# Performance work log

Measured on AMD Instinct MI355X. Metric: run time of the kernel, lower is better.

Reference implementation:

```python
import jax, jax.numpy as jnp
import numpy as np

N = 50000      # nodes per graph batch (per siamese side)
E = 500000     # edges per side
F_IN = 128     # input_channels
H = 128        # hidden_channels
OUT = 2        # output_channels
G = 512        # number of graphs in the batch


def setup_inputs() -> dict:
    key = jax.random.key(0)
    ks = jax.random.split(key, 16)

    def lin_w(k, fan_in, shape):
        lim = 1.0 / np.sqrt(fan_in)
        return jax.random.uniform(k, shape, jnp.float32, -lim, lim)

    return {
        "x1": jax.random.normal(ks[0], (N, F_IN), jnp.float32),
        "x2": jax.random.normal(ks[1], (N, F_IN), jnp.float32),
        "edge_index1": jax.random.randint(ks[2], (2, E), 0, N, jnp.int32),
        "edge_index2": jax.random.randint(ks[3], (2, E), 0, N, jnp.int32),
        "batch1": jnp.sort(jax.random.randint(ks[4], (N,), 0, G, jnp.int32)),
        "batch2": jnp.sort(jax.random.randint(ks[5], (N,), 0, G, jnp.int32)),
        "W1": lin_w(ks[6], F_IN, (F_IN, H)), "b1": jnp.zeros((H,), jnp.float32),
        "W2": lin_w(ks[7], H, (H, H)),       "b2": jnp.zeros((H,), jnp.float32),
        "W3": lin_w(ks[8], H, (H, H)),       "b3": jnp.zeros((H,), jnp.float32),
        "Wc1": lin_w(ks[9], 2 * H, (2 * H, 4 * H)), "bc1": jnp.zeros((4 * H,), jnp.float32),
        "Wc2": lin_w(ks[10], 4 * H, (4 * H, 2 * H)), "bc2": jnp.zeros((2 * H,), jnp.float32),
        "Wc3": lin_w(ks[11], 2 * H, (2 * H, OUT)),   "bc3": jnp.zeros((OUT,), jnp.float32),
        "num_graphs": G,
    }


def _gcn_layer(x, W, b, src, dst, dinv):
    # PyG GCNConv: linear transform, then deg^{-1/2} A_hat deg^{-1/2} aggregation + bias
    h = x @ W
    msg = h[src] * (dinv[src] * dinv[dst])[:, None]   # [E+N, H]
    return jax.ops.segment_sum(msg, dst, num_segments=x.shape[0]) + b


def _forward_once(x, edge_index, batch, W1, b1, W2, b2, W3, b3, num_graphs):
    n = x.shape[0]
    loop = jnp.arange(n, dtype=edge_index.dtype)
    src = jnp.concatenate([edge_index[0], loop])      # add self-loops
    dst = jnp.concatenate([edge_index[1], loop])
    deg = jax.ops.segment_sum(jnp.ones_like(dst, dtype=x.dtype), dst, num_segments=n)
    dinv = jax.lax.rsqrt(deg)                          # deg >= 1 due to self-loops
    h = jax.nn.relu(_gcn_layer(x, W1, b1, src, dst, dinv))
    h = jax.nn.relu(_gcn_layer(h, W2, b2, src, dst, dinv))
    h = _gcn_layer(h, W3, b3, src, dst, dinv)
    # global_mean_pool over batch indices
    s = jax.ops.segment_sum(h, batch, num_segments=num_graphs)
    cnt = jax.ops.segment_sum(jnp.ones((n,), x.dtype), batch, num_segments=num_graphs)
    return s / jnp.maximum(cnt, 1.0)[:, None]


def reference(x1, x2, edge_index1, edge_index2, batch1, batch2,
              W1, b1, W2, b2, W3, b3, Wc1, bc1, Wc2, bc2, Wc3, bc3, num_graphs):
    g1 = _forward_once(x1, edge_index1, batch1, W1, b1, W2, b2, W3, b3, num_graphs)
    g2 = _forward_once(x2, edge_index2, batch2, W1, b1, W2, b2, W3, b3, num_graphs)
    z = jnp.concatenate([g1, g2], axis=1)             # [G, 2H]
    z = jax.nn.relu(z @ Wc1 + bc1)
    z = jax.nn.relu(z @ Wc2 + bc2)
    # dropout p=0.5 is identity at eval time
    return z @ Wc3 + bc3                               # [G, OUT]
```

## Files before the change

### kernel.cpp

```cpp
#include <hip/hip_runtime.h>
#include <math.h>

#define N_NODES 50000
#define E_EDGES 500000
#define HDIM    128
#define OUTC    2
#define NGRAPH  512

typedef _Float16 f16x8 __attribute__((ext_vector_type(8)));
typedef float    f32x4 __attribute__((ext_vector_type(4)));

__global__ void k_prep(const float* __restrict__ W1, const float* __restrict__ W2,
                       _Float16* __restrict__ w1hi, _Float16* __restrict__ w1lo,
                       _Float16* __restrict__ w2hi, _Float16* __restrict__ w2lo) {
    int i = blockIdx.x * blockDim.x + threadIdx.x;
    int stride = gridDim.x * blockDim.x;
    for (int j = i; j < 128 * 128; j += stride) {
        int n = j >> 7, k = j & 127;
        float v = W1[k * 128 + n];
        _Float16 h = (_Float16)v;
        w1hi[j] = h; w1lo[j] = (_Float16)(v - (float)h);
        v = W2[k * 128 + n];
        h = (_Float16)v;
        w2hi[j] = h; w2lo[j] = (_Float16)(v - (float)h);
    }
}

__global__ void k_hist(const int* __restrict__ d0, const int* __restrict__ d1,
                       int ecnt, int off1, int* __restrict__ cnt) {
    int i = blockIdx.x * blockDim.x + threadIdx.x;
    int stride = gridDim.x * blockDim.x;
    for (; i < ecnt; i += stride) {
        int d = (i < E_EDGES) ? d0[i] : d1[i - E_EDGES] + off1;
        atomicAdd(&cnt[d], 1);
    }
}

__global__ void k_scan_a(const int* __restrict__ cnt, int* __restrict__ excl,
                         int* __restrict__ blksum, float* __restrict__ dinv,
                         const int* __restrict__ bt0, const int* __restrict__ bt1,
                         int goff0, int nn, int nside, float* __restrict__ cnt_g) {
    __shared__ int s[512];
    int t = threadIdx.x;
    int i = blockIdx.x * 512 + t;
    int v = 0;
    if (i < nn) {
        v = cnt[i];
        dinv[i] = 1.0f / sqrtf((float)(v + 1));
        int g = (i < nside) ? bt0[i] + goff0 : bt1[i - nside] + NGRAPH;
        atomicAdd(&cnt_g[g], 1.0f);
    }
    s[t] = v; __syncthreads();
    for (int off = 1; off < 512; off <<= 1) {
        int add = (t >= off) ? s[t - off] : 0;
        __syncthreads();
        s[t] += add;
        __syncthreads();
    }
    if (i < nn) excl[i] = s[t] - v;
    if (t == 511) blksum[blockIdx.x] = s[511];
}

__global__ void k_scan_b(int* __restrict__ blksum, int nb) {
    __shared__ int s[512];
    int t = threadIdx.x;
    int v = (t < nb) ? blksum[t] : 0;
    s[t] = v; __syncthreads();
    for (int off = 1; off < 512; off <<= 1) {
        int add = (t >= off) ? s[t - off] : 0;
        __syncthreads();
        s[t] += add;
        __syncthreads();
    }
    if (t < nb) blksum[t] = s[t] - v;
}

__global__ void k_scan_c(int* __restrict__ excl, const int* __restrict__ blksum,
                         int* __restrict__ cursor, int nn, int tot) {
    int t = threadIdx.x;
    int i = blockIdx.x * 512 + t;
    if (i < nn) {
        int v = excl[i] + blksum[blockIdx.x];
        excl[i] = v;
        cursor[i] = v;
    }
    if (i == 0) excl[nn] = tot;
}

__global__ void k_fill(const int* __restrict__ s0, const int* __restrict__ s1,
                       const int* __restrict__ d0, const int* __restrict__ d1,
                       int ecnt, int off1, int goff0,
                       const int* __restrict__ bt0, const int* __restrict__ bt1,
                       int* __restrict__ cursor,
                       const float* __restrict__ dinv, int2* __restrict__ edges,
                       int* __restrict__ gdst) {
    int i = blockIdx.x * blockDim.x + threadIdx.x;
    int stride = gridDim.x * blockDim.x;
    for (; i < ecnt; i += stride) {
        int d, sg, g;
        if (i < E_EDGES) {
            int dl = d0[i];
            sg = s0[i]; d = dl; g = bt0[dl] + goff0;
        } else {
            int dl = d1[i - E_EDGES];
            sg = s1[i - E_EDGES] + off1; d = dl + off1; g = bt1[dl] + NGRAPH;
        }
        int p = atomicAdd(&cursor[d], 1);
        float w = dinv[sg] * dinv[d];
        edges[p] = make_int2(sg, __float_as_int(w));
        gdst[p] = g;
    }
}

__device__ inline void cvt8(const float4& p, const float4& q, f16x8& h, f16x8& l) {
    float v[8] = {p.x, p.y, p.z, p.w, q.x, q.y, q.z, q.w};
#pragma unroll
    for (int i = 0; i < 8; i++) {
        _Float16 hh = (_Float16)v[i];
        h[i] = hh;
        l[i] = (_Float16)(v[i] - (float)hh);
    }
}

template <int ASRC>
__global__ __launch_bounds__(256) void k_gemm_split(
        const float* __restrict__ A0f, const float* __restrict__ A1f, int nside,
        const _Float16* __restrict__ Ahi, const _Float16* __restrict__ Alo,
        const _Float16* __restrict__ Bhi, const _Float16* __restrict__ Blo,
        float* __restrict__ C, int M) {
    __shared__ _Float16 sA[2][128][40];
    __shared__ _Float16 sB[2][128][40];
    int tid = threadIdx.x;
    int wave = tid >> 6, lane = tid & 63;
    int wm = (wave >> 1) * 64;
    int wn = (wave & 1) * 64;
    int quad = lane >> 4, fm = lane & 15;
    int row0 = blockIdx.x * 128;

    int lr = tid >> 2;
    int lk = (tid & 3) * 8;

    f32x4 acc[4][4] = {};
    const float4 z4 = make_float4(0.f, 0.f, 0.f, 0.f);

    for (int kc = 0; kc < 128; kc += 32) {
        int r1 = row0 + lr, r2 = row0 + lr + 64;
        bool ok1 = r1 < M, ok2 = r2 < M;
        f16x8 ah1, al1, ah2, al2;
        if (ASRC == 1) {
            const float* p1 = (r1 < nside) ? A0f + (size_t)r1 * 128
                                           : A1f + (size_t)(r1 - nside) * 128;
            const float* p2 = (r2 < nside) ? A0f + (size_t)r2 * 128
                                           : A1f + (size_t)(r2 - nside) * 128;
            float4 a = ok1 ? *(const float4*)(p1 + kc + lk) : z4;
            float4 b = ok1 ? *(const float4*)(p1 + kc + lk + 4) : z4;
            float4 c = ok2 ? *(const float4*)(p2 + kc + lk) : z4;
            float4 d = ok2 ? *(const float4*)(p2 + kc + lk + 4) : z4;
            cvt8(a, b, ah1, al1);
            cvt8(c, d, ah2, al2);
        } else {
            const f16x8 zf = {};
            ah1 = ok1 ? *(const f16x8*)(Ahi + (size_t)r1 * 128 + kc + lk) : zf;
            al1 = ok1 ? *(const f16x8*)(Alo + (size_t)r1 * 128 + kc + lk) : zf;
            ah2 = ok2 ? *(const f16x8*)(Ahi + (size_t)r2 * 128 + kc + lk) : zf;
            al2 = ok2 ? *(const f16x8*)(Alo + (size_t)r2 * 128 + kc + lk) : zf;
        }
        f16x8 bh1 = *(const f16x8*)(Bhi + (size_t)lr * 128 + kc + lk);
        f16x8 bl1 = *(const f16x8*)(Blo + (size_t)lr * 128 + kc + lk);
        f16x8 bh2 = *(const f16x8*)(Bhi + (size_t)(lr + 64) * 128 + kc + lk);
        f16x8 bl2 = *(const f16x8*)(Blo + (size_t)(lr + 64) * 128 + kc + lk);
        __syncthreads();
        *(f16x8*)&sA[0][lr][lk]      = ah1;
        *(f16x8*)&sA[1][lr][lk]      = al1;
        *(f16x8*)&sA[0][lr + 64][lk] = ah2;
        *(f16x8*)&sA[1][lr + 64][lk] = al2;
        *(f16x8*)&sB[0][lr][lk]      = bh1;
        *(f16x8*)&sB[1][lr][lk]      = bl1;
        *(f16x8*)&sB[0][lr + 64][lk] = bh2;
        *(f16x8*)&sB[1][lr + 64][lk] = bl2;
        __syncthreads();

        f16x8 afh[4], afl[4], bfh[4], bfl[4];
#pragma unroll
        for (int mi = 0; mi < 4; mi++) {
            afh[mi] = *(const f16x8*)&sA[0][wm + mi * 16 + fm][quad * 8];
            afl[mi] = *(const f16x8*)&sA[1][wm + mi * 16 + fm][quad * 8];
        }
#pragma unroll
        for (int ni = 0; ni < 4; ni++) {
            bfh[ni] = *(const f16x8*)&sB[0][wn + ni * 16 + fm][quad * 8];
            bfl[ni] = *(const f16x8*)&sB[1][wn + ni * 16 + fm][quad * 8];
        }
#pragma unroll
        for (int mi = 0; mi < 4; mi++)
#pragma unroll
            for (int ni = 0; ni < 4; ni++) {
                acc[mi][ni] = __builtin_amdgcn_mfma_f32_16x16x32_f16(afh[mi], bfh[ni], acc[mi][ni], 0, 0, 0);
                acc[mi][ni] = __builtin_amdgcn_mfma_f32_16x16x32_f16(afh[mi], bfl[ni], acc[mi][ni], 0, 0, 0);
                acc[mi][ni] = __builtin_amdgcn_mfma_f32_16x16x32_f16(afl[mi], bfh[ni], acc[mi][ni], 0, 0, 0);
            }
    }

#pragma unroll
    for (int mi = 0; mi < 4; mi++)
#pragma unroll
        for (int reg = 0; reg < 4; reg++) {
            int r = row0 + wm + mi * 16 + quad * 4 + reg;
            if (r >= M) continue;
#pragma unroll
            for (int ni = 0; ni < 4; ni++)
                C[(size_t)r * 128 + wn + ni * 16 + fm] = acc[mi][ni][reg];
        }
}

__global__ __launch_bounds__(256) void k_gemm(
        const float* __restrict__ A, const float* __restrict__ B,
        const float* __restrict__ bias, float* __restrict__ C,
        int M, int Nn, int K, int ldc, int act) {
    __shared__ float As[16][64];
    __shared__ float Bs[16][68];
    int tid = threadIdx.x;
    int tx = tid & 15, ty = tid >> 4;
    int row0 = blockIdx.x * 64, col0 = blockIdx.y * 64;
    float acc[4][4] = {};
    int arow = tid >> 2;
    int acol = (tid & 3) * 4;
    int brow = tid >> 4;
    int bcol = (tid & 15) * 4;

    for (int k0 = 0; k0 < K; k0 += 16) {
        float4 av = make_float4(0.f, 0.f, 0.f, 0.f);
        int ar = row0 + arow;
        if (ar < M) av = *(const float4*)(A + (size_t)ar * K + k0 + acol);
        As[acol + 0][arow] = av.x;
        As[acol + 1][arow] = av.y;
        As[acol + 2][arow] = av.z;
        As[acol + 3][arow] = av.w;

        float4 bv = make_float4(0.f, 0.f, 0.f, 0.f);
        const float* Brow = B + (size_t)(k0 + brow) * Nn;
        int bc = col0 + bcol;
        if (bc + 3 < Nn) {
            bv = *(const float4*)(Brow + bc);
        } else {
            if (bc     < Nn) bv.x = Brow[bc];
            if (bc + 1 < Nn) bv.y = Brow[bc + 1];
            if (bc + 2 < Nn) bv.z = Brow[bc + 2];
        }
        Bs[brow][bcol + 0] = bv.x;
        Bs[brow][bcol + 1] = bv.y;
        Bs[brow][bcol + 2] = bv.z;
        Bs[brow][bcol + 3] = bv.w;
        __syncthreads();

#pragma unroll
        for (int k = 0; k < 16; k++) {
            float4 a = *(const float4*)&As[k][ty * 4];
            float4 b = *(const float4*)&Bs[k][tx * 4];
            acc[0][0] += a.x * b.x; acc[0][1] += a.x * b.y; acc[0][2] += a.x * b.z; acc[0][3] += a.x * b.w;
            acc[1][0] += a.y * b.x; acc[1][1] += a.y * b.y; acc[1][2] += a.y * b.z; acc[1][3] += a.y * b.w;
            acc[2][0] += a.z * b.x; acc[2][1] += a.z * b.y; acc[2][2] += a.z * b.z; acc[2][3] += a.z * b.w;
            acc[3][0] += a.w * b.x; acc[3][1] += a.w * b.y; acc[3][2] += a.w * b.z; acc[3][3] += a.w * b.w;
        }
        __syncthreads();
    }

#pragma unroll
    for (int i = 0; i < 4; i++) {
        int r = row0 + ty * 4 + i;
        if (r >= M) continue;
#pragma unroll
        for (int j = 0; j < 4; j++) {
            int c = col0 + tx * 4 + j;
            if (c >= Nn) continue;
            float v = acc[i][j];
            if (bias) v += bias[c];
            if (act) v = fmaxf(v, 0.0f);
            C[(size_t)r * ldc + c] = v;
        }
    }
}

__global__ __launch_bounds__(256) void k_gemm_pool(
        const float* __restrict__ pool, const float* __restrict__ cnt_g,
        const float* __restrict__ W, const float* __restrict__ bias,
        float* __restrict__ zcat) {
    __shared__ float As[16][64];
    __shared__ float Bs[16][68];
    int side = blockIdx.z;
    const float* A = pool + (size_t)side * NGRAPH * HDIM;
    const float* cg = cnt_g + side * NGRAPH;
    int tid = threadIdx.x;
    int tx = tid & 15, ty = tid >> 4;
    int row0 = blockIdx.x * 64, col0 = blockIdx.y * 64;
    float acc[4][4] = {};
    int arow = tid >> 2;
    int acol = (tid & 3) * 4;
    int brow = tid >> 4;
    int bcol = (tid & 15) * 4;

    for (int k0 = 0; k0 < 128; k0 += 16) {
        int ar = row0 + arow;
        float sc = 1.0f / fmaxf(cg[ar], 1.0f);
        float4 av = *(const float4*)(A + (size_t)ar * 128 + k0 + acol);
        As[acol + 0][arow] = av.x * sc;
        As[acol + 1][arow] = av.y * sc;
        As[acol + 2][arow] = av.z * sc;
        As[acol + 3][arow] = av.w * sc;

        float4 bv = *(const float4*)(W + (size_t)(k0 + brow) * 128 + col0 + bcol);
        Bs[brow][bcol + 0] = bv.x;
        Bs[brow][bcol + 1] = bv.y;
        Bs[brow][bcol + 2] = bv.z;
        Bs[brow][bcol + 3] = bv.w;
        __syncthreads();

#pragma unroll
        for (int k = 0; k < 16; k++) {
            float4 a = *(const float4*)&As[k][ty * 4];
            float4 b = *(const float4*)&Bs[k][tx * 4];
            acc[0][0] += a.x * b.x; acc[0][1] += a.x * b.y; acc[0][2] += a.x * b.z; acc[0][3] += a.x * b.w;
            acc[1][0] += a.y * b.x; acc[1][1] += a.y * b.y; acc[1][2] += a.y * b.z; acc[1][3] += a.y * b.w;
            acc[2][0] += a.z * b.x; acc[2][1] += a.z * b.y; acc[2][2] += a.z * b.z; acc[2][3] += a.z * b.w;
            acc[3][0] += a.w * b.x; acc[3][1] += a.w * b.y; acc[3][2] += a.w * b.z; acc[3][3] += a.w * b.w;
        }
        __syncthreads();
    }

#pragma unroll
    for (int i = 0; i < 4; i++) {
        int r = row0 + ty * 4 + i;
#pragma unroll
        for (int j = 0; j < 4; j++) {
            int c = col0 + tx * 4 + j;
            zcat[(size_t)r * 256 + side * 128 + c] = acc[i][j] + bias[c];
        }
    }
}

template <int PACK>
__global__ __launch_bounds__(256) void k_agg(
        const float* __restrict__ H, const float* __restrict__ dinv,
        const int* __restrict__ row_ptr, const int2* __restrict__ edges,
        const float* __restrict__ bias,
        _Float16* __restrict__ outHi, _Float16* __restrict__ outLo,
        float* __restrict__ outF, int nnodes) {
    int wave = threadIdx.x >> 6, lane = threadIdx.x & 63;
    int node = blockIdx.x * 4 + wave;
    if (node >= nnodes) return;

    float di = dinv[node];
    float2 hv = ((const float2*)(H + (size_t)node * HDIM))[lane];
    float wself = di * di;
    float ax = hv.x * wself;
    float ay = hv.y * wself;

    int rs = __builtin_amdgcn_readfirstlane(row_ptr[node]);
    int re = __builtin_amdgcn_readfirstlane(row_ptr[node + 1]);

    for (int base = rs; base < re; base += 8) {
        int nrem = re - base, m = nrem - 1;
        int i1 = 1 < nrem ? 1 : m;
        int i2 = 2 < nrem ? 2 : m;
        int i3 = 3 < nrem ? 3 : m;
        int i4 = 4 < nrem ? 4 : m;
        int i5 = 5 < nrem ? 5 : m;
        int i6 = 6 < nrem ? 6 : m;
        int i7 = 7 < nrem ? 7 : m;
        int2 E0 = edges[base];
        int2 E1 = edges[base + i1];
        int2 E2 = edges[base + i2];
        int2 E3 = edges[base + i3];
        int2 E4 = edges[base + i4];
        int2 E5 = edges[base + i5];
        int2 E6 = edges[base + i6];
        int2 E7 = edges[base + i7];
        float2 v0 = ((const float2*)(H + (size_t)E0.x * HDIM))[lane];
        float2 v1 = ((const float2*)(H + (size_t)E1.x * HDIM))[lane];
        float2 v2 = ((const float2*)(H + (size_t)E2.x * HDIM))[lane];
        float2 v3 = ((const float2*)(H + (size_t)E3.x * HDIM))[lane];
        float2 v4 = ((const float2*)(H + (size_t)E4.x * HDIM))[lane];
        float2 v5 = ((const float2*)(H + (size_t)E5.x * HDIM))[lane];
        float2 v6 = ((const float2*)(H + (size_t)E6.x * HDIM))[lane];
        float2 v7 = ((const float2*)(H + (size_t)E7.x * HDIM))[lane];
        float w0 = __int_as_float(E0.y);
        float w1 = 1 < nrem ? __int_as_float(E1.y) : 0.f;
        float w2 = 2 < nrem ? __int_as_float(E2.y) : 0.f;
        float w3 = 3 < nrem ? __int_as_float(E3.y) : 0.f;
        float w4 = 4 < nrem ? __int_as_float(E4.y) : 0.f;
        float w5 = 5 < nrem ? __int_as_float(E5.y) : 0.f;
        float w6 = 6 < nrem ? __int_as_float(E6.y) : 0.f;
        float w7 = 7 < nrem ? __int_as_float(E7.y) : 0.f;
        ax = fmaf(v0.x, w0, ax); ay = fmaf(v0.y, w0, ay);
        ax = fmaf(v1.x, w1, ax); ay = fmaf(v1.y, w1, ay);
        ax = fmaf(v2.x, w2, ax); ay = fmaf(v2.y, w2, ay);
        ax = fmaf(v3.x, w3, ax); ay = fmaf(v3.y, w3, ay);
        ax = fmaf(v4.x, w4, ax); ay = fmaf(v4.y, w4, ay);
        ax = fmaf(v5.x, w5, ax); ay = fmaf(v5.y, w5, ay);
        ax = fmaf(v6.x, w6, ax); ay = fmaf(v6.y, w6, ay);
        ax = fmaf(v7.x, w7, ax); ay = fmaf(v7.y, w7, ay);
    }

    float ox = fmaxf(ax + bias[lane * 2],     0.0f);
    float oy = fmaxf(ay + bias[lane * 2 + 1], 0.0f);
    if (PACK) {
        _Float16 hx = (_Float16)ox, hy = (_Float16)oy;
        _Float16 lx = (_Float16)(ox - (float)hx), ly = (_Float16)(oy - (float)hy);
        union { _Float16 h[2]; unsigned u; } ph, pl;
        ph.h[0] = hx; ph.h[1] = hy;
        pl.h[0] = lx; pl.h[1] = ly;
        ((unsigned*)(outHi + (size_t)node * HDIM))[lane] = ph.u;
        ((unsigned*)(outLo + (size_t)node * HDIM))[lane] = pl.u;
    } else {
        ((float2*)(outF + (size_t)node * HDIM))[lane] = make_float2(ox, oy);
    }
}

__global__ __launch_bounds__(256) void k_sweep3(
        const float* __restrict__ H, const int2* __restrict__ edges,
        const int* __restrict__ gdst, const float* __restrict__ dinv,
        const int* __restrict__ bt0, const int* __restrict__ bt1,
        int goff0, int nnodes, int nside, int nedges,
        float* __restrict__ pool) {
    int lane = threadIdx.x & 63;
    int wid = blockIdx.x * 4 + (threadIdx.x >> 6);
    int ewaves = (nedges + 63) >> 6;

    float ax = 0.f, ay = 0.f;

    if (wid < ewaves) {
        int e0 = wid << 6;
        int e1 = e0 + 64; if (e1 > nedges) e1 = nedges;
        int gcur = __builtin_amdgcn_readfirstlane(gdst[e0]);
        for (int base = e0; base < e1; base += 8) {
            int nrem = e1 - base, m = nrem - 1;
            int i1 = 1 < nrem ? 1 : m;
            int i2 = 2 < nrem ? 2 : m;
            int i3 = 3 < nrem ? 3 : m;
            int i4 = 4 < nrem ? 4 : m;
            int i5 = 5 < nrem ? 5 : m;
            int i6 = 6 < nrem ? 6 : m;
            int i7 = 7 < nrem ? 7 : m;
            int2 E0 = edges[base];
            int2 E1 = edges[base + i1];
            int2 E2 = edges[base + i2];
            int2 E3 = edges[base + i3];
            int2 E4 = edges[base + i4];
            int2 E5 = edges[base + i5];
            int2 E6 = edges[base + i6];
            int2 E7 = edges[base + i7];
            int g0 = __builtin_amdgcn_readfirstlane(gdst[base]);
            int g1 = __builtin_amdgcn_readfirstlane(gdst[base + i1]);
            int g2 = __builtin_amdgcn_readfirstlane(gdst[base + i2]);
            int g3 = __builtin_amdgcn_readfirstlane(gdst[base + i3]);
            int g4 = __builtin_amdgcn_readfirstlane(gdst[base + i4]);
            int g5 = __builtin_amdgcn_readfirstlane(gdst[base + i5]);
            int g6 = __builtin_amdgcn_readfirstlane(gdst[base + i6]);
            int g7 = __builtin_amdgcn_readfirstlane(gdst[base + i7]);
            float2 v0 = ((const float2*)(H + (size_t)E0.x * HDIM))[lane];
            float2 v1 = ((const float2*)(H + (size_t)E1.x * HDIM))[lane];
            float2 v2 = ((const float2*)(H + (size_t)E2.x * HDIM))[lane];
            float2 v3 = ((const float2*)(H + (size_t)E3.x * HDIM))[lane];
            float2 v4 = ((const float2*)(H + (size_t)E4.x * HDIM))[lane];
            float2 v5 = ((const float2*)(H + (size_t)E5.x * HDIM))[lane];
            float2 v6 = ((const float2*)(H + (size_t)E6.x * HDIM))[lane];
            float2 v7 = ((const float2*)(H + (size_t)E7.x * HDIM))[lane];
            float w0 = __int_as_float(E0.y);
            float w1 = 1 < nrem ? __int_as_float(E1.y) : 0.f;
            float w2 = 2 < nrem ? __int_as_float(E2.y) : 0.f;
            float w3 = 3 < nrem ? __int_as_float(E3.y) : 0.f;
            float w4 = 4 < nrem ? __int_as_float(E4.y) : 0.f;
            float w5 = 5 < nrem ? __int_as_float(E5.y) : 0.f;
            float w6 = 6 < nrem ? __int_as_float(E6.y) : 0.f;
            float w7 = 7 < nrem ? __int_as_float(E7.y) : 0.f;

            if ((g0 | g1 | g2 | g3 | g4 | g5 | g6 | g7) ==
                (g0 & g1 & g2 & g3 & g4 & g5 & g6 & g7) && g0 == gcur) {
                ax = fmaf(v0.x, w0, ax); ay = fmaf(v0.y, w0, ay);
                ax = fmaf(v1.x, w1, ax); ay = fmaf(v1.y, w1, ay);
                ax = fmaf(v2.x, w2, ax); ay = fmaf(v2.y, w2, ay);
                ax = fmaf(v3.x, w3, ax); ay = fmaf(v3.y, w3, ay);
                ax = fmaf(v4.x, w4, ax); ay = fmaf(v4.y, w4, ay);
                ax = fmaf(v5.x, w5, ax); ay = fmaf(v5.y, w5, ay);
                ax = fmaf(v6.x, w6, ax); ay = fmaf(v6.y, w6, ay);
                ax = fmaf(v7.x, w7, ax); ay = fmaf(v7.y, w7, ay);
            } else {
                int   gg[8] = {g0, g1, g2, g3, g4, g5, g6, g7};
                float wx[8] = {w0, w1, w2, w3, w4, w5, w6, w7};
                float2 vv[8] = {v0, v1, v2, v3, v4, v5, v6, v7};
#pragma unroll
                for (int j = 0; j < 8; j++) {
                    if (wx[j] != 0.f && gg[j] != gcur) {
                        float* p = pool + (size_t)gcur * HDIM + lane * 2;
                        atomicAdd(p, ax); atomicAdd(p + 1, ay);
                        ax = 0.f; ay = 0.f;
                        gcur = gg[j];
                    }
                    ax = fmaf(vv[j].x, wx[j], ax);
                    ay = fmaf(vv[j].y, wx[j], ay);
                }
            }
        }
        float* p = pool + (size_t)gcur * HDIM + lane * 2;
        atomicAdd(p, ax); atomicAdd(p + 1, ay);
    } else {
        int wid2 = wid - ewaves;
        int n0 = wid2 << 6;
        if (n0 >= nnodes) return;
        int n1 = n0 + 64; if (n1 > nnodes) n1 = nnodes;
        int gcur = (n0 < nside) ? bt0[n0] + goff0 : bt1[n0 - nside] + NGRAPH;
        gcur = __builtin_amdgcn_readfirstlane(gcur);
        for (int n = n0; n < n1; n++) {
            int g = (n < nside) ? bt0[n] + goff0 : bt1[n - nside] + NGRAPH;
            g = __builtin_amdgcn_readfirstlane(g);
            float dn = dinv[n];
            float w = dn * dn;
            float2 v = ((const float2*)(H + (size_t)n * HDIM))[lane];
            if (g != gcur) {
                float* p = pool + (size_t)gcur * HDIM + lane * 2;
                atomicAdd(p, ax); atomicAdd(p + 1, ay);
                ax = 0.f; ay = 0.f;
                gcur = g;
            }
            ax = fmaf(v.x, w, ax);
            ay = fmaf(v.y, w, ay);
        }
        float* p = pool + (size_t)gcur * HDIM + lane * 2;
        atomicAdd(p, ax); atomicAdd(p + 1, ay);
    }
}

extern "C" void kernel_launch(void* const* d_in, const int* in_sizes, int n_in,
                              void* d_out, int out_size, void* d_ws, size_t ws_size,
                              hipStream_t stream) {
    (void)in_sizes; (void)n_in; (void)out_size;

    const float* x[2]  = {(const float*)d_in[0], (const float*)d_in[1]};
    const int*   ei[2] = {(const int*)d_in[2], (const int*)d_in[3]};
    const int*   bt[2] = {(const int*)d_in[4], (const int*)d_in[5]};
    const float* W1  = (const float*)d_in[6];  const float* b1  = (const float*)d_in[7];
    const float* W2  = (const float*)d_in[8];  const float* b2  = (const float*)d_in[9];
    const float* W3  = (const float*)d_in[10]; const float* b3  = (const float*)d_in[11];
    const float* Wc1 = (const float*)d_in[12]; const float* bc1 = (const float*)d_in[13];
    const float* Wc2 = (const float*)d_in[14]; const float* bc2 = (const float*)d_in[15];
    const float* Wc3 = (const float*)d_in[16]; const float* bc3 = (const float*)d_in[17];
    float* out = (float*)d_out;

    const bool batched = ws_size >= 120ull * 1000 * 1000;
    const int NN = batched ? 2 * N_NODES : N_NODES;
    const int NE = batched ? 2 * E_EDGES : E_EDGES;

    char* ws = (char*)d_ws;
    size_t off = 0;
    auto carve = [&](size_t bytes) -> char* {
        char* p = ws + off;
        off += (bytes + 255) & ~(size_t)255;
        return p;
    };

    int*   edge_cnt = (int*)  carve((size_t)NN * 4);
    int*   cursor   = (int*)  carve((size_t)NN * 4);
    float* pool_s   = (float*)carve((size_t)2 * NGRAPH * HDIM * 4);
    float* cnt_g    = (float*)carve((size_t)2 * NGRAPH * 4);
    float* dinv     = (float*)carve((size_t)NN * 4);
    int*   row_ptr  = (int*)  carve((size_t)(NN + 1) * 4);
    int2*  edges    = (int2*) carve((size_t)NE * 8);
    int*   gdst     = (int*)  carve((size_t)NE * 4);
    int*   blksum   = (int*)  carve(1024 * 4);
    _Float16* wt    = (_Float16*)carve(4 * 128 * 128 * 2);
    _Float16* hS    = (_Float16*)carve((size_t)NN * HDIM * 4);
    float* hA       = (float*)carve((size_t)NN * HDIM * 4);
    float* zcat     = (float*)carve((size_t)NGRAPH * 2 * HDIM * 4);
    float* z1       = (float*)carve((size_t)NGRAPH * 4 * HDIM * 4);
    float* z2       = (float*)carve((size_t)NGRAPH * 2 * HDIM * 4);

    _Float16* w1hi = wt;
    _Float16* w1lo = wt + 128 * 128;
    _Float16* w2hi = wt + 2 * 128 * 128;
    _Float16* w2lo = wt + 3 * 128 * 128;
    _Float16* hShi = hS;
    _Float16* hSlo = hS + (size_t)NN * HDIM;
    float*    hSf  = (float*)hS;

    const int gblk = (NN + 127) / 128;
    const size_t poolz = (size_t)2 * NGRAPH * HDIM * 4 + (size_t)2 * NGRAPH * 4;

    hipMemsetAsync(pool_s, 0, poolz, stream);
    k_prep<<<64, 256, 0, stream>>>(W1, W2, w1hi, w1lo, w2hi, w2lo);

    if (batched) {
        const int nscan = (2 * N_NODES + 511) / 512;
        const int ablk  = (2 * N_NODES + 3) / 4;
        const int swaves = ((2 * E_EDGES + 63) >> 6) + ((2 * N_NODES + 63) >> 6);
        const int sblk = (swaves + 3) / 4;

        hipMemsetAsync(edge_cnt, 0, (size_t)NN * 4, stream);
        k_hist<<<1024, 256, 0, stream>>>(ei[0] + E_EDGES, ei[1] + E_EDGES,
                                         2 * E_EDGES, N_NODES, edge_cnt);
        k_scan_a<<<nscan, 512, 0, stream>>>(edge_cnt, row_ptr, blksum, dinv,
                                            bt[0], bt[1], 0, 2 * N_NODES, N_NODES, cnt_g);
        k_scan_b<<<1, 512, 0, stream>>>(blksum, nscan);
        k_scan_c<<<nscan, 512, 0, stream>>>(row_ptr, blksum, cursor, 2 * N_NODES, 2 * E_EDGES);
        k_fill<<<1024, 256, 0, stream>>>(ei[0], ei[1], ei[0] + E_EDGES, ei[1] + E_EDGES,
                                         2 * E_EDGES, N_NODES, 0, bt[0], bt[1],
                                         cursor, dinv, edges, gdst);

        k_gemm_split<1><<<gblk, 256, 0, stream>>>(x[0], x[1], N_NODES,
                                                  nullptr, nullptr, w1hi, w1lo, hA, 2 * N_NODES);
        k_agg<1><<<ablk, 256, 0, stream>>>(hA, dinv, row_ptr, edges, b1,
                                           hShi, hSlo, nullptr, 2 * N_NODES);
        k_gemm_split<0><<<gblk, 256, 0, stream>>>(nullptr, nullptr, 0,
                                                  hShi, hSlo, w2hi, w2lo, hA, 2 * N_NODES);
        k_agg<0><<<ablk, 256, 0, stream>>>(hA, dinv, row_ptr, edges, b2,
                                           nullptr, nullptr, hSf, 2 * N_NODES);
        k_sweep3<<<sblk, 256, 0, stream>>>(hSf, edges, gdst, dinv, bt[0], bt[1],
                                           0, 2 * N_NODES, N_NODES, 2 * E_EDGES, pool_s);
    } else {
        const int nscan = (N_NODES + 511) / 512;
        const int ablk  = (N_NODES + 3) / 4;
        const int swaves = ((E_EDGES + 63) >> 6) + ((N_NODES + 63) >> 6);
        const int sblk = (swaves + 3) / 4;

        for (int s = 0; s < 2; ++s) {
            const int* esrc = ei[s];
            const int* edst = ei[s] + E_EDGES;
            int goff = s * NGRAPH;

            hipMemsetAsync(edge_cnt, 0, (size_t)NN * 4, stream);
            k_hist<<<512, 256, 0, stream>>>(edst, edst, E_EDGES, 0, edge_cnt);
            k_scan_a<<<nscan, 512, 0, stream>>>(edge_cnt, row_ptr, blksum, dinv,
                                                bt[s], bt[s], goff, N_NODES, N_NODES, cnt_g);
            k_scan_b<<<1, 512, 0, stream>>>(blksum, nscan);
            k_scan_c<<<nscan, 512, 0, stream>>>(row_ptr, blksum, cursor, N_NODES, E_EDGES);
            k_fill<<<512, 256, 0, stream>>>(esrc, esrc, edst, edst, E_EDGES, 0, goff,
                                            bt[s], bt[s], cursor, dinv, edges, gdst);

            k_gemm_split<1><<<gblk, 256, 0, stream>>>(x[s], x[s], N_NODES,
                                                      nullptr, nullptr, w1hi, w1lo, hA, N_NODES);
            k_agg<1><<<ablk, 256, 0, stream>>>(hA, dinv, row_ptr, edges, b1,
                                               hShi, hSlo, nullptr, N_NODES);
            k_gemm_split<0><<<gblk, 256, 0, stream>>>(nullptr, nullptr, 0,
                                                      hShi, hSlo, w2hi, w2lo, hA, N_NODES);
            k_agg<0><<<ablk, 256, 0, stream>>>(hA, dinv, row_ptr, edges, b2,
                                               nullptr, nullptr, hSf, N_NODES);
            k_sweep3<<<sblk, 256, 0, stream>>>(hSf, edges, gdst, dinv, bt[s], bt[s],
                                               goff, N_NODES, N_NODES, E_EDGES, pool_s);
        }
    }

    k_gemm_pool<<<dim3(NGRAPH / 64, 2, 2), 256, 0, stream>>>(pool_s, cnt_g, W3, b3, zcat);

    k_gemm<<<dim3(NGRAPH / 64, (4 * HDIM) / 64), 256, 0, stream>>>(zcat, Wc1, bc1, z1, NGRAPH, 4 * HDIM, 2 * HDIM, 4 * HDIM, 1);
    k_gemm<<<dim3(NGRAPH / 64, (2 * HDIM) / 64), 256, 0, stream>>>(z1, Wc2, bc2, z2, NGRAPH, 2 * HDIM, 4 * HDIM, 2 * HDIM, 1);
    k_gemm<<<dim3(NGRAPH / 64, 1), 256, 0, stream>>>(z2, Wc3, bc3, out, NGRAPH, OUTC, 2 * HDIM, OUTC, 0);
}
```

Measured before the change: 678.3 us.

## Use half-wave float4 gathers in aggregation and fuse weight prep into histogram

The aggregation and layer-3 sweep kernels now split each wave into two halves that gather two different source rows at once using float4 loads, then combine the halves with a cross-lane shuffle. This processes 16 edges per loop iteration and aims to get more gathers in flight per wave. The weight-split prep is folded into the histogram kernel, and the pool, count and edge-count memsets are merged into a single contiguous memset, which removes launches. The trade-offs are extra shuffle work, a serial one-edge-at-a-time fallback in the sweep whenever a 64-edge chunk crosses a graph boundary, and a dependence on the buffers lying contiguously in memory.

```diff
diff --git a/kernel.cpp b/kernel.cpp
--- a/kernel.cpp
+++ b/kernel.cpp
@@ -10,7 +10,9 @@
 typedef _Float16 f16x8 __attribute__((ext_vector_type(8)));
 typedef float    f32x4 __attribute__((ext_vector_type(4)));
 
-__global__ void k_prep(const float* __restrict__ W1, const float* __restrict__ W2,
+__global__ void k_hist(const int* __restrict__ d0, const int* __restrict__ d1,
+                       int ecnt, int off1, int* __restrict__ cnt,
+                       const float* __restrict__ W1, const float* __restrict__ W2,
                        _Float16* __restrict__ w1hi, _Float16* __restrict__ w1lo,
                        _Float16* __restrict__ w2hi, _Float16* __restrict__ w2lo) {
     int i = blockIdx.x * blockDim.x + threadIdx.x;
@@ -24,14 +26,8 @@
         h = (_Float16)v;
         w2hi[j] = h; w2lo[j] = (_Float16)(v - (float)h);
     }
-}
-
-__global__ void k_hist(const int* __restrict__ d0, const int* __restrict__ d1,
-                       int ecnt, int off1, int* __restrict__ cnt) {
-    int i = blockIdx.x * blockDim.x + threadIdx.x;
-    int stride = gridDim.x * blockDim.x;
-    for (; i < ecnt; i += stride) {
-        int d = (i < E_EDGES) ? d0[i] : d1[i - E_EDGES] + off1;
+    for (int j = i; j < ecnt; j += stride) {
+        int d = (j < E_EDGES) ? d0[j] : d1[j - E_EDGES] + off1;
         atomicAdd(&cnt[d], 1);
     }
 }
@@ -346,73 +342,64 @@
         _Float16* __restrict__ outHi, _Float16* __restrict__ outLo,
         float* __restrict__ outF, int nnodes) {
     int wave = threadIdx.x >> 6, lane = threadIdx.x & 63;
+    int half = lane >> 5, li = lane & 31;
     int node = blockIdx.x * 4 + wave;
     if (node >= nnodes) return;
 
     float di = dinv[node];
-    float2 hv = ((const float2*)(H + (size_t)node * HDIM))[lane];
-    float wself = di * di;
-    float ax = hv.x * wself;
-    float ay = hv.y * wself;
+    float4 hv = ((const float4*)(H + (size_t)node * HDIM))[li];
+    float wself = half ? 0.f : di * di;
+    float4 acc;
+    acc.x = hv.x * wself; acc.y = hv.y * wself;
+    acc.z = hv.z * wself; acc.w = hv.w * wself;
 
     int rs = __builtin_amdgcn_readfirstlane(row_ptr[node]);
     int re = __builtin_amdgcn_readfirstlane(row_ptr[node + 1]);
 
-    for (int base = rs; base < re; base += 8) {
+    for (int base = rs; base < re; base += 16) {
         int nrem = re - base, m = nrem - 1;
-        int i1 = 1 < nrem ? 1 : m;
-        int i2 = 2 < nrem ? 2 : m;
-        int i3 = 3 < nrem ? 3 : m;
-        int i4 = 4 < nrem ? 4 : m;
-        int i5 = 5 < nrem ? 5 : m;
-        int i6 = 6 < nrem ? 6 : m;
-        int i7 = 7 < nrem ? 7 : m;
-        int2 E0 = edges[base];
-        int2 E1 = edges[base + i1];
-        int2 E2 = edges[base + i2];
-        int2 E3 = edges[base + i3];
-        int2 E4 = edges[base + i4];
-        int2 E5 = edges[base + i5];
-        int2 E6 = edges[base + i6];
-        int2 E7 = edges[base + i7];
-        float2 v0 = ((const float2*)(H + (size_t)E0.x * HDIM))[lane];
-        float2 v1 = ((const float2*)(H + (size_t)E1.x * HDIM))[lane];
-        float2 v2 = ((const float2*)(H + (size_t)E2.x * HDIM))[lane];
-        float2 v3 = ((const float2*)(H + (size_t)E3.x * HDIM))[lane];
-        float2 v4 = ((const float2*)(H + (size_t)E4.x * HDIM))[lane];
-        float2 v5 = ((const float2*)(H + (size_t)E5.x * HDIM))[lane];
-        float2 v6 = ((const float2*)(H + (size_t)E6.x * HDIM))[lane];
-        float2 v7 = ((const float2*)(H + (size_t)E7.x * HDIM))[lane];
-        float w0 = __int_as_float(E0.y);
-        float w1 = 1 < nrem ? __int_as_float(E1.y) : 0.f;
-        float w2 = 2 < nrem ? __int_as_float(E2.y) : 0.f;
-        float w3 = 3 < nrem ? __int_as_float(E3.y) : 0.f;
-        float w4 = 4 < nrem ? __int_as_float(E4.y) : 0.f;
-        float w5 = 5 < nrem ? __int_as_float(E5.y) : 0.f;
-        float w6 = 6 < nrem ? __int_as_float(E6.y) : 0.f;
-        float w7 = 7 < nrem ? __int_as_float(E7.y) : 0.f;
-        ax = fmaf(v0.x, w0, ax); ay = fmaf(v0.y, w0, ay);
-        ax = fmaf(v1.x, w1, ax); ay = fmaf(v1.y, w1, ay);
-        ax = fmaf(v2.x, w2, ax); ay = fmaf(v2.y, w2, ay);
-        ax = fmaf(v3.x, w3, ax); ay = fmaf(v3.y, w3, ay);
-        ax = fmaf(v4.x, w4, ax); ay = fmaf(v4.y, w4, ay);
-        ax = fmaf(v5.x, w5, ax); ay = fmaf(v5.y, w5, ay);
-        ax = fmaf(v6.x, w6, ax); ay = fmaf(v6.y, w6, ay);
-        ax = fmaf(v7.x, w7, ax); ay = fmaf(v7.y, w7, ay);
-    }
-
-    float ox = fmaxf(ax + bias[lane * 2],     0.0f);
-    float oy = fmaxf(ay + bias[lane * 2 + 1], 0.0f);
-    if (PACK) {
-        _Float16 hx = (_Float16)ox, hy = (_Float16)oy;
-        _Float16 lx = (_Float16)(ox - (float)hx), ly = (_Float16)(oy - (float)hy);
-        union { _Float16 h[2]; unsigned u; } ph, pl;
-        ph.h[0] = hx; ph.h[1] = hy;
-        pl.h[0] = lx; pl.h[1] = ly;
-        ((unsigned*)(outHi + (size_t)node * HDIM))[lane] = ph.u;
-        ((unsigned*)(outLo + (size_t)node * HDIM))[lane] = pl.u;
-    } else {
-        ((float2*)(outF + (size_t)node * HDIM))[lane] = make_float2(ox, oy);
+        int2 R[16];
+#pragma unroll
+        for (int j = 0; j < 16; j++)
+            R[j] = edges[base + (j < nrem ? j : m)];
+#pragma unroll
+        for (int j = 0; j < 8; j++) {
+            int srcj = half ? R[2 * j + 1].x : R[2 * j].x;
+            int wbit = half ? R[2 * j + 1].y : R[2 * j].y;
+            float wj = (2 * j + half) < nrem ? __int_as_float(wbit) : 0.f;
+            float4 v = ((const float4*)(H + (size_t)srcj * HDIM))[li];
+            acc.x = fmaf(v.x, wj, acc.x);
+            acc.y = fmaf(v.y, wj, acc.y);
+            acc.z = fmaf(v.z, wj, acc.z);
+            acc.w = fmaf(v.w, wj, acc.w);
+        }
+    }
+
+    acc.x += __shfl_xor(acc.x, 32);
+    acc.y += __shfl_xor(acc.y, 32);
+    acc.z += __shfl_xor(acc.z, 32);
+    acc.w += __shfl_xor(acc.w, 32);
+
+    if (half == 0) {
+        float4 b = ((const float4*)bias)[li];
+        float o0 = fmaxf(acc.x + b.x, 0.f);
+        float o1 = fmaxf(acc.y + b.y, 0.f);
+        float o2 = fmaxf(acc.z + b.z, 0.f);
+        float o3 = fmaxf(acc.w + b.w, 0.f);
+        if (PACK) {
+            float o[4] = {o0, o1, o2, o3};
+            union { _Float16 h[4]; uint2 u; } ph, pl;
+#pragma unroll
+            for (int i = 0; i < 4; i++) {
+                _Float16 hh = (_Float16)o[i];
+                ph.h[i] = hh;
+                pl.h[i] = (_Float16)(o[i] - (float)hh);
+            }
+            ((uint2*)(outHi + (size_t)node * HDIM))[li] = ph.u;
+            ((uint2*)(outLo + (size_t)node * HDIM))[li] = pl.u;
+        } else {
+            ((float4*)(outF + (size_t)node * HDIM))[li] = make_float4(o0, o1, o2, o3);
+        }
     }
 }
 
@@ -423,91 +410,68 @@
         int goff0, int nnodes, int nside, int nedges,
         float* __restrict__ pool) {
     int lane = threadIdx.x & 63;
+    int half = lane >> 5, li = lane & 31;
     int wid = blockIdx.x * 4 + (threadIdx.x >> 6);
     int ewaves = (nedges + 63) >> 6;
-
-    float ax = 0.f, ay = 0.f;
 
     if (wid < ewaves) {
         int e0 = wid << 6;
         int e1 = e0 + 64; if (e1 > nedges) e1 = nedges;
-        int gcur = __builtin_amdgcn_readfirstlane(gdst[e0]);
-        for (int base = e0; base < e1; base += 8) {
-            int nrem = e1 - base, m = nrem - 1;
-            int i1 = 1 < nrem ? 1 : m;
-            int i2 = 2 < nrem ? 2 : m;
-            int i3 = 3 < nrem ? 3 : m;
-            int i4 = 4 < nrem ? 4 : m;
-            int i5 = 5 < nrem ? 5 : m;
-            int i6 = 6 < nrem ? 6 : m;
-            int i7 = 7 < nrem ? 7 : m;
-            int2 E0 = edges[base];
-            int2 E1 = edges[base + i1];
-            int2 E2 = edges[base + i2];
-            int2 E3 = edges[base + i3];
-            int2 E4 = edges[base + i4];
-            int2 E5 = edges[base + i5];
-            int2 E6 = edges[base + i6];
-            int2 E7 = edges[base + i7];
-            int g0 = __builtin_amdgcn_readfirstlane(gdst[base]);
-            int g1 = __builtin_amdgcn_readfirstlane(gdst[base + i1]);
-            int g2 = __builtin_amdgcn_readfirstlane(gdst[base + i2]);
-            int g3 = __builtin_amdgcn_readfirstlane(gdst[base + i3]);
-            int g4 = __builtin_amdgcn_readfirstlane(gdst[base + i4]);
-            int g5 = __builtin_amdgcn_readfirstlane(gdst[base + i5]);
-            int g6 = __builtin_amdgcn_readfirstlane(gdst[base + i6]);
-            int g7 = __builtin_amdgcn_readfirstlane(gdst[base + i7]);
-            float2 v0 = ((const float2*)(H + (size_t)E0.x * HDIM))[lane];
-            float2 v1 = ((const float2*)(H + (size_t)E1.x * HDIM))[lane];
-            float2 v2 = ((const float2*)(H + (size_t)E2.x * HDIM))[lane];
-            float2 v3 = ((const float2*)(H + (size_t)E3.x * HDIM))[lane];
-            float2 v4 = ((const float2*)(H + (size_t)E4.x * HDIM))[lane];
-            float2 v5 = ((const float2*)(H + (size_t)E5.x * HDIM))[lane];
-            float2 v6 = ((const float2*)(H + (size_t)E6.x * HDIM))[lane];
-            float2 v7 = ((const float2*)(H + (size_t)E7.x * HDIM))[lane];
-            float w0 = __int_as_float(E0.y);
-            float w1 = 1 < nrem ? __int_as_float(E1.y) : 0.f;
-            float w2 = 2 < nrem ? __int_as_float(E2.y) : 0.f;
-            float w3 = 3 < nrem ? __int_as_float(E3.y) : 0.f;
-            float w4 = 4 < nrem ? __int_as_float(E4.y) : 0.f;
-            float w5 = 5 < nrem ? __int_as_float(E5.y) : 0.f;
-            float w6 = 6 < nrem ? __int_as_float(E6.y) : 0.f;
-            float w7 = 7 < nrem ? __int_as_float(E7.y) : 0.f;
-
-            if ((g0 | g1 | g2 | g3 | g4 | g5 | g6 | g7) ==
-                (g0 & g1 & g2 & g3 & g4 & g5 & g6 & g7) && g0 == gcur) {
-                ax = fmaf(v0.x, w0, ax); ay = fmaf(v0.y, w0, ay);
-                ax = fmaf(v1.x, w1, ax); ay = fmaf(v1.y, w1, ay);
-                ax = fmaf(v2.x, w2, ax); ay = fmaf(v2.y, w2, ay);
-                ax = fmaf(v3.x, w3, ax); ay = fmaf(v3.y, w3, ay);
-                ax = fmaf(v4.x, w4, ax); ay = fmaf(v4.y, w4, ay);
-                ax = fmaf(v5.x, w5, ax); ay = fmaf(v5.y, w5, ay);
-                ax = fmaf(v6.x, w6, ax); ay = fmaf(v6.y, w6, ay);
-                ax = fmaf(v7.x, w7, ax); ay = fmaf(v7.y, w7, ay);
-            } else {
-                int   gg[8] = {g0, g1, g2, g3, g4, g5, g6, g7};
-                float wx[8] = {w0, w1, w2, w3, w4, w5, w6, w7};
-                float2 vv[8] = {v0, v1, v2, v3, v4, v5, v6, v7};
+        int gfirst = __builtin_amdgcn_readfirstlane(gdst[e0]);
+        int glast  = __builtin_amdgcn_readfirstlane(gdst[e1 - 1]);
+        float4 acc = make_float4(0.f, 0.f, 0.f, 0.f);
+
+        if (gfirst == glast) {
+            for (int base = e0; base < e1; base += 16) {
+                int nrem = e1 - base, m = nrem - 1;
+                int2 R[16];
+#pragma unroll
+                for (int j = 0; j < 16; j++)
+                    R[j] = edges[base + (j < nrem ? j : m)];
 #pragma unroll
                 for (int j = 0; j < 8; j++) {
-                    if (wx[j] != 0.f && gg[j] != gcur) {
-                        float* p = pool + (size_t)gcur * HDIM + lane * 2;
-                        atomicAdd(p, ax); atomicAdd(p + 1, ay);
-                        ax = 0.f; ay = 0.f;
-                        gcur = gg[j];
-                    }
-                    ax = fmaf(vv[j].x, wx[j], ax);
-                    ay = fmaf(vv[j].y, wx[j], ay);
+                    int srcj = half ? R[2 * j + 1].x : R[2 * j].x;
+                    int wbit = half ? R[2 * j + 1].y : R[2 * j].y;
+                    float wj = (2 * j + half) < nrem ? __int_as_float(wbit) : 0.f;
+                    float4 v = ((const float4*)(H + (size_t)srcj * HDIM))[li];
+                    acc.x = fmaf(v.x, wj, acc.x);
+                    acc.y = fmaf(v.y, wj, acc.y);
+                    acc.z = fmaf(v.z, wj, acc.z);
+                    acc.w = fmaf(v.w, wj, acc.w);
                 }
             }
-        }
-        float* p = pool + (size_t)gcur * HDIM + lane * 2;
-        atomicAdd(p, ax); atomicAdd(p + 1, ay);
+            float* p = pool + (size_t)gfirst * HDIM + li * 4;
+            atomicAdd(p + 0, acc.x); atomicAdd(p + 1, acc.y);
+            atomicAdd(p + 2, acc.z); atomicAdd(p + 3, acc.w);
+        } else {
+            int gcur = gfirst;
+            for (int e = e0; e < e1; e++) {
+                int2 E = edges[e];
+                int g = __builtin_amdgcn_readfirstlane(gdst[e]);
+                if (g != gcur) {
+                    float* p = pool + (size_t)gcur * HDIM + li * 4;
+                    atomicAdd(p + 0, acc.x); atomicAdd(p + 1, acc.y);
+                    atomicAdd(p + 2, acc.z); atomicAdd(p + 3, acc.w);
+                    acc = make_float4(0.f, 0.f, 0.f, 0.f);
+                    gcur = g;
+                }
+                float wj = half ? 0.f : __int_as_float(E.y);
+                float4 v = ((const float4*)(H + (size_t)E.x * HDIM))[li];
+                acc.x = fmaf(v.x, wj, acc.x);
+                acc.y = fmaf(v.y, wj, acc.y);
+                acc.z = fmaf(v.z, wj, acc.z);
+                acc.w = fmaf(v.w, wj, acc.w);
+            }
+            float* p = pool + (size_t)gcur * HDIM + li * 4;
+            atomicAdd(p + 0, acc.x); atomicAdd(p + 1, acc.y);
+            atomicAdd(p + 2, acc.z); atomicAdd(p + 3, acc.w);
+        }
     } else {
         int wid2 = wid - ewaves;
         int n0 = wid2 << 6;
         if (n0 >= nnodes) return;
         int n1 = n0 + 64; if (n1 > nnodes) n1 = nnodes;
+        float ax = 0.f, ay = 0.f;
         int gcur = (n0 < nside) ? bt0[n0] + goff0 : bt1[n0 - nside] + NGRAPH;
         gcur = __builtin_amdgcn_readfirstlane(gcur);
         for (int n = n0; n < n1; n++) {
@@ -583,10 +547,8 @@
     float*    hSf  = (float*)hS;
 
     const int gblk = (NN + 127) / 128;
-    const size_t poolz = (size_t)2 * NGRAPH * HDIM * 4 + (size_t)2 * NGRAPH * 4;
-
-    hipMemsetAsync(pool_s, 0, poolz, stream);
-    k_prep<<<64, 256, 0, stream>>>(W1, W2, w1hi, w1lo, w2hi, w2lo);
+    size_t zero_all = (size_t)((char*)cnt_g + 2 * NGRAPH * 4 - (char*)edge_cnt);
+    size_t zero_cnt = (size_t)((char*)pool_s - (char*)edge_cnt);
 
     if (batched) {
         const int nscan = (2 * N_NODES + 511) / 512;
@@ -594,9 +556,10 @@
         const int swaves = ((2 * E_EDGES + 63) >> 6) + ((2 * N_NODES + 63) >> 6);
         const int sblk = (swaves + 3) / 4;
 
-        hipMemsetAsync(edge_cnt, 0, (size_t)NN * 4, stream);
+        hipMemsetAsync(edge_cnt, 0, zero_all, stream);
         k_hist<<<1024, 256, 0, stream>>>(ei[0] + E_EDGES, ei[1] + E_EDGES,
-                                         2 * E_EDGES, N_NODES, edge_cnt);
+                                         2 * E_EDGES, N_NODES, edge_cnt,
+                                         W1, W2, w1hi, w1lo, w2hi, w2lo);
         k_scan_a<<<nscan, 512, 0, stream>>>(edge_cnt, row_ptr, blksum, dinv,
                                             bt[0], bt[1], 0, 2 * N_NODES, N_NODES, cnt_g);
         k_scan_b<<<1, 512, 0, stream>>>(blksum, nscan);
@@ -626,8 +589,9 @@
             const int* edst = ei[s] + E_EDGES;
             int goff = s * NGRAPH;
 
-            hipMemsetAsync(edge_cnt, 0, (size_t)NN * 4, stream);
-            k_hist<<<512, 256, 0, stream>>>(edst, edst, E_EDGES, 0, edge_cnt);
+            hipMemsetAsync(edge_cnt, 0, s == 0 ? zero_all : zero_cnt, stream);
+            k_hist<<<512, 256, 0, stream>>>(edst, edst, E_EDGES, 0, edge_cnt,
+                                            W1, W2, w1hi, w1lo, w2hi, w2lo);
             k_scan_a<<<nscan, 512, 0, stream>>>(edge_cnt, row_ptr, blksum, dinv,
                                                 bt[s], bt[s], goff, N_NODES, N_NODES, cnt_g);
             k_scan_b<<<1, 512, 0, stream>>>(blksum, nscan);
```

After: 1.081 ms. 59.4% more time.
